# Kernel tuning notes

Measured on AMD Instinct MI355X. Metric: run time of the kernel, lower is better.

Reference implementation:

```python
import jax, jax.numpy as jnp
import numpy as np

NY, NU, NHIDDEN = 64, 64, 256
NHRZ, NBATCH = 1024, 128


def setup_inputs() -> dict:
    key = jax.random.key(0)
    ks = jax.random.split(key, 9)
    y0 = jax.random.normal(ks[0], (NBATCH, NY), dtype=jnp.float32)
    U = jax.random.normal(ks[1], (NHRZ, NBATCH, NU), dtype=jnp.float32)
    # parameters (match torch init: uniform(0,1) for continuous eigen params,
    # randn/sqrt(Nu) for B, Kaiming-uniform-ish for Linear layers)
    lmbd_cont_real = jax.random.uniform(ks[2], (NHIDDEN // 2,), dtype=jnp.float32)
    lmbd_cont_imag = jax.random.uniform(ks[3], (NHIDDEN // 2,), dtype=jnp.float32)
    B = jax.random.normal(ks[4], (NHIDDEN, NU), dtype=jnp.float32) / np.sqrt(NU)
    lim1 = 1.0 / np.sqrt(NY)
    W_y2x = jax.random.uniform(ks[5], (NHIDDEN, NY), dtype=jnp.float32, minval=-lim1, maxval=lim1)
    b_y2x = jax.random.uniform(ks[6], (NHIDDEN,), dtype=jnp.float32, minval=-lim1, maxval=lim1)
    lim2 = 1.0 / np.sqrt(NHIDDEN)
    W_x2y = jax.random.uniform(ks[7], (NY, NHIDDEN), dtype=jnp.float32, minval=-lim2, maxval=lim2)
    b_x2y = jax.random.uniform(ks[8], (NY,), dtype=jnp.float32, minval=-lim2, maxval=lim2)
    return {"y0": y0, "U": U, "lmbd_cont_real": lmbd_cont_real,
            "lmbd_cont_imag": lmbd_cont_imag, "B": B,
            "W_y2x": W_y2x, "b_y2x": b_y2x, "W_x2y": W_x2y, "b_x2y": b_x2y}


def reference(y0, U, lmbd_cont_real, lmbd_cont_imag, B, W_y2x, b_y2x, W_x2y, b_x2y):
    n = lmbd_cont_real.shape[0]  # Nhidden // 2
    r = jnp.exp(-jnp.abs(lmbd_cont_real))
    theta = (np.pi / 2.0) * lmbd_cont_imag
    lmbd_real = r * jnp.cos(theta)  # [n]
    lmbd_imag = r * jnp.sin(theta)  # [n]
    nf = jnp.sqrt(1.0 - jnp.exp(-2.0 * jnp.abs(lmbd_cont_real)))
    nf = jnp.concatenate([nf, nf])  # [Nhidden]
    # Bu[t,b,h] = (U @ B^T) * nf
    Bu = jnp.einsum('tbu,hu->tbh', U, B) * nf  # [Nhrz, Nbatch, Nhidden]
    x0 = y0 @ W_y2x.T + b_y2x  # [Nbatch, Nhidden]

    # x @ A^T with A = [[diag(lr), -diag(li)], [diag(li), diag(lr)]] is a
    # per-pair 2x2 rotation -> pure elementwise ops (same math, no dense matmul)
    def step(x, bu):
        x1, x2 = x[:, :n], x[:, n:]
        xn = jnp.concatenate([lmbd_real * x1 - lmbd_imag * x2,
                              lmbd_imag * x1 + lmbd_real * x2], axis=-1) + bu
        return xn, xn

    _, X = jax.lax.scan(step, x0, Bu)  # X: [Nhrz, Nbatch, Nhidden]
    Y = X @ W_x2y.T + b_x2y  # [Nhrz, Nbatch, Ny]
    return Y
```

## Files before the change

kernel.cpp:

```cpp
#include <hip/hip_runtime.h>
#include <hip/hip_bf16.h>
#include <stdint.h>

#define T_HRZ 1024
#define NBAT  128
#define NHID  256
#define NPAIR 128
#define NUIN  64
#define NYOUT 64
#define LCH   16
#define CCH   64

#define WS_LAM   0
#define WS_LAML  256
#define WS_X0P   512
#define WS_WBU   33280
#define WS_WBY   41472
#define WS_S     49664
#define WS_E     2146816

#define X16_PITCH 264
#define XA_SB 136
#define XA_SK 552

typedef __attribute__((ext_vector_type(8))) short short8;
typedef __attribute__((ext_vector_type(4))) float float4v;

union Frag { short8 s8; unsigned int u32[4]; };

__device__ __forceinline__ unsigned int f2bf_bits(float x) {
  unsigned int u = __float_as_uint(x);
  return (u + 0x7fffu + ((u >> 16) & 1u)) >> 16;
}

__device__ __forceinline__ unsigned int pkbf(float a, float b) {
  __hip_bfloat162 h = __float22bfloat162_rn(make_float2(a, b));
  union { __hip_bfloat162 h2; unsigned int u; } cv; cv.h2 = h; return cv.u;
}

__global__ __launch_bounds__(256) void k_prep(
    const float* __restrict__ y0, const float* __restrict__ lrc,
    const float* __restrict__ lic, const float* __restrict__ Bm,
    const float* __restrict__ Wy2x, const float* __restrict__ by2x,
    const float* __restrict__ Wx2y, float* __restrict__ ws)
{
  int blk = blockIdx.x;
  int h = threadIdx.x;
  if (blk < NBAT) {
    __shared__ float y0s[NYOUT];
    if (h < NYOUT) y0s[h] = y0[blk * NYOUT + h];
    __syncthreads();
    float acc = by2x[h];
    const float* wr = Wy2x + h * NYOUT;
#pragma unroll 16
    for (int k = 0; k < NYOUT; ++k) acc += y0s[k] * wr[k];
    int j = h & (NPAIR - 1);
    int comp = h >> 7;
    ws[WS_X0P + (blk * NPAIR + j) * 2 + comp] = acc;
  } else if (blk == NBAT) {
    if (h < NPAIR) {
      float a  = fabsf(lrc[h]);
      float r  = expf(-a);
      float th = 1.5707963267948966f * lic[h];
      float lr = r * cosf(th);
      float li = r * sinf(th);
      ws[WS_LAM + h]         = lr;
      ws[WS_LAM + NPAIR + h] = li;
      float pr = lr, pi_ = li;
      for (int l = 1; l < LCH; ++l) {
        float nr = pr * lr - pi_ * li;
        float ni = pr * li + pi_ * lr;
        pr = nr; pi_ = ni;
      }
      ws[WS_LAML + h]         = pr;
      ws[WS_LAML + NPAIR + h] = pi_;
    }
  } else if (blk == NBAT + 1) {
    unsigned short* wbu = (unsigned short*)(ws + WS_WBU);
    for (int idx = h; idx < 16384; idx += 256) {
      int nt   = idx >> 10;
      int kk   = (idx >> 9) & 1;
      int lane = (idx >> 3) & 63;
      int jj   = idx & 7;
      int u  = kk * 32 + (lane >> 4) * 8 + jj;
      int hh = nt * 16 + (lane & 15);
      float a2 = fabsf(lrc[hh & (NPAIR - 1)]);
      float nf = sqrtf(1.f - expf(-2.f * a2));
      wbu[idx] = (unsigned short)f2bf_bits(Bm[hh * NUIN + u] * nf);
    }
  } else {
    unsigned short* wby = (unsigned short*)(ws + WS_WBY);
    for (int idx = h; idx < 16384; idx += 256) {
      int nt   = idx >> 12;
      int kk   = (idx >> 9) & 7;
      int lane = (idx >> 3) & 63;
      int jj   = idx & 7;
      int hh = kk * 32 + (lane >> 4) * 8 + jj;
      int y  = nt * 16 + (lane & 15);
      wby[idx] = (unsigned short)f2bf_bits(Wx2y[y * NHID + hh]);
    }
  }
}

__global__ __launch_bounds__(128, 6) void k_phaseA(
    const float* __restrict__ U, float* __restrict__ ws)
{
  int b = blockIdx.x, c = blockIdx.y;
  int tid = threadIdx.x, wave = tid >> 6, lane = tid & 63;
  int l15 = lane & 15, q = lane >> 4;
  __shared__ unsigned short X16[LCH * X16_PITCH];

  const float* urow = U + ((size_t)(c * LCH + l15) * NBAT + b) * NUIN;
  Frag afr[2];
#pragma unroll
  for (int kk = 0; kk < 2; ++kk) {
    int u0 = kk * 32 + q * 8;
    float4 va = *(const float4*)(urow + u0);
    float4 vb = *(const float4*)(urow + u0 + 4);
    afr[kk].u32[0] = pkbf(va.x, va.y);
    afr[kk].u32[1] = pkbf(va.z, va.w);
    afr[kk].u32[2] = pkbf(vb.x, vb.y);
    afr[kk].u32[3] = pkbf(vb.z, vb.w);
  }

  const short8* wbu = (const short8*)(ws + WS_WBU);
  float4v z = {0.f, 0.f, 0.f, 0.f};
  float4v acc[8];
#pragma unroll
  for (int n = 0; n < 8; ++n) acc[n] = z;
#pragma unroll
  for (int n = 0; n < 8; ++n) {
    int nt = wave * 8 + n;
    acc[n] = __builtin_amdgcn_mfma_f32_16x16x32_bf16(afr[0].s8, wbu[(nt * 2 + 0) * 64 + lane], acc[n], 0, 0, 0);
    acc[n] = __builtin_amdgcn_mfma_f32_16x16x32_bf16(afr[1].s8, wbu[(nt * 2 + 1) * 64 + lane], acc[n], 0, 0, 0);
  }

#pragma unroll
  for (int n = 0; n < 8; ++n) {
    int hh = (wave * 8 + n) * 16 + l15;
    int off = (hh & 127) * 2 + (hh >> 7);
#pragma unroll
    for (int r = 0; r < 4; ++r)
      X16[(q * 4 + r) * X16_PITCH + off] = (unsigned short)f2bf_bits(acc[n][r]);
  }
  __syncthreads();

  int j = tid;
  float lr = ws[WS_LAM + j], li = ws[WS_LAM + NPAIR + j];
  unsigned int pk[LCH];
#pragma unroll
  for (int l = 0; l < LCH; ++l)
    pk[l] = *(const unsigned int*)(X16 + l * X16_PITCH + j * 2);
  float s1 = 0.f, s2 = 0.f;
#pragma unroll
  for (int l = 0; l < LCH; ++l) {
    float v1 = __uint_as_float(pk[l] << 16);
    float v2 = __uint_as_float(pk[l] & 0xffff0000u);
    float n1 = lr * s1 - li * s2 + v1;
    float n2 = li * s1 + lr * s2 + v2;
    s1 = n1; s2 = n2;
  }
  ((float2*)(ws + WS_S))[((size_t)c * NBAT + b) * NPAIR + j] = make_float2(s1, s2);
}

__global__ __launch_bounds__(128) void k_phaseB(float* __restrict__ ws)
{
  int b = blockIdx.x, j = threadIdx.x;
  float e1 = ws[WS_X0P + (b * NPAIR + j) * 2 + 0];
  float e2 = ws[WS_X0P + (b * NPAIR + j) * 2 + 1];
  float Lr = ws[WS_LAML + j], Li = ws[WS_LAML + NPAIR + j];
  const float2* sp = (const float2*)(ws + WS_S);
  float2* ep = (float2*)(ws + WS_E);
  const size_t cs = (size_t)NBAT * NPAIR;
  size_t o0 = (size_t)b * NPAIR + j;
  float2 buf[8];
#pragma unroll
  for (int k = 0; k < 8; ++k) buf[k] = sp[k * cs + o0];
  for (int g = 0; g < 8; ++g) {
    float2 nxt[8];
    if (g < 7) {
#pragma unroll
      for (int k = 0; k < 8; ++k) nxt[k] = sp[(size_t)((g + 1) * 8 + k) * cs + o0];
    }
#pragma unroll
    for (int k = 0; k < 8; ++k) {
      ep[(size_t)(g * 8 + k) * cs + o0] = make_float2(e1, e2);
      float n1 = Lr * e1 - Li * e2 + buf[k].x;
      float n2 = Li * e1 + Lr * e2 + buf[k].y;
      e1 = n1; e2 = n2;
    }
    if (g < 7) {
#pragma unroll
      for (int k = 0; k < 8; ++k) buf[k] = nxt[k];
    }
  }
}

__global__ __launch_bounds__(128, 4) void k_phaseC(
    const float* __restrict__ U, const float* __restrict__ bx2y,
    float* __restrict__ out, float* __restrict__ ws)
{
  int b = blockIdx.x, c = blockIdx.y;
  int tid = threadIdx.x, wave = tid >> 6, lane = tid & 63;
  int l15 = lane & 15, q = lane >> 4;
  __shared__ unsigned short X16[LCH * X16_PITCH];
  __shared__ unsigned short XA[8 * XA_SK];

  int j = tid;
  float lr = ws[WS_LAM + j], li = ws[WS_LAM + NPAIR + j];
  float2 e = ((const float2*)(ws + WS_E))[((size_t)c * NBAT + b) * NPAIR + j];

  const float* urow = U + ((size_t)(c * LCH + l15) * NBAT + b) * NUIN;
  Frag afr[2];
#pragma unroll
  for (int kk = 0; kk < 2; ++kk) {
    int u0 = kk * 32 + q * 8;
    float4 va = *(const float4*)(urow + u0);
    float4 vb = *(const float4*)(urow + u0 + 4);
    afr[kk].u32[0] = pkbf(va.x, va.y);
    afr[kk].u32[1] = pkbf(va.z, va.w);
    afr[kk].u32[2] = pkbf(vb.x, vb.y);
    afr[kk].u32[3] = pkbf(vb.z, vb.w);
  }

  const short8* wbu = (const short8*)(ws + WS_WBU);
  float4v z = {0.f, 0.f, 0.f, 0.f};
  {
    float4v acc[8];
#pragma unroll
    for (int n = 0; n < 8; ++n) acc[n] = z;
#pragma unroll
    for (int n = 0; n < 8; ++n) {
      int nt = wave * 8 + n;
      acc[n] = __builtin_amdgcn_mfma_f32_16x16x32_bf16(afr[0].s8, wbu[(nt * 2 + 0) * 64 + lane], acc[n], 0, 0, 0);
      acc[n] = __builtin_amdgcn_mfma_f32_16x16x32_bf16(afr[1].s8, wbu[(nt * 2 + 1) * 64 + lane], acc[n], 0, 0, 0);
    }
#pragma unroll
    for (int n = 0; n < 8; ++n) {
      int hh = (wave * 8 + n) * 16 + l15;
      int off = (hh & 127) * 2 + (hh >> 7);
#pragma unroll
      for (int r = 0; r < 4; ++r)
        X16[(q * 4 + r) * X16_PITCH + off] = (unsigned short)f2bf_bits(acc[n][r]);
    }
  }
  __syncthreads();

  unsigned int pk[LCH];
#pragma unroll
  for (int l = 0; l < LCH; ++l)
    pk[l] = *(const unsigned int*)(X16 + l * X16_PITCH + j * 2);

  int base1 = (j >> 5) * XA_SK       + ((j >> 3) & 3) * XA_SB + (j & 7);
  int base2 = ((j >> 5) + 4) * XA_SK + ((j >> 3) & 3) * XA_SB + (j & 7);
  float x1 = e.x, x2 = e.y;
#pragma unroll
  for (int l = 0; l < LCH; ++l) {
    float v1 = __uint_as_float(pk[l] << 16);
    float v2 = __uint_as_float(pk[l] & 0xffff0000u);
    float n1 = lr * x1 - li * x2 + v1;
    float n2 = li * x1 + lr * x2 + v2;
    x1 = n1; x2 = n2;
    XA[base1 + l * 8] = (unsigned short)f2bf_bits(x1);
    XA[base2 + l * 8] = (unsigned short)f2bf_bits(x2);
  }
  __syncthreads();

  const short8* wby = (const short8*)(ws + WS_WBY);
  float4v acc0 = z, acc1 = z;
  int nt0 = wave * 2, nt1 = nt0 + 1;
#pragma unroll
  for (int kk = 0; kk < 8; ++kk) {
    short8 a = *(const short8*)(XA + kk * XA_SK + q * XA_SB + l15 * 8);
    acc0 = __builtin_amdgcn_mfma_f32_16x16x32_bf16(a, wby[(nt0 * 8 + kk) * 64 + lane], acc0, 0, 0, 0);
    acc1 = __builtin_amdgcn_mfma_f32_16x16x32_bf16(a, wby[(nt1 * 8 + kk) * 64 + lane], acc1, 0, 0, 0);
  }

  float bias0 = bx2y[nt0 * 16 + l15];
  float bias1 = bx2y[nt1 * 16 + l15];
#pragma unroll
  for (int r = 0; r < 4; ++r) {
    int row = q * 4 + r;
    size_t o = ((size_t)(c * LCH + row) * NBAT + b) * NYOUT;
    out[o + nt0 * 16 + l15] = acc0[r] + bias0;
    out[o + nt1 * 16 + l15] = acc1[r] + bias1;
  }
}

extern "C" void kernel_launch(void* const* d_in, const int* in_sizes, int n_in,
                              void* d_out, int out_size, void* d_ws, size_t ws_size,
                              hipStream_t stream) {
  (void)in_sizes; (void)n_in; (void)out_size; (void)ws_size;
  const float* y0   = (const float*)d_in[0];
  const float* U    = (const float*)d_in[1];
  const float* lrc  = (const float*)d_in[2];
  const float* lic  = (const float*)d_in[3];
  const float* Bm   = (const float*)d_in[4];
  const float* Wy2x = (const float*)d_in[5];
  const float* by2x = (const float*)d_in[6];
  const float* Wx2y = (const float*)d_in[7];
  const float* bx2y = (const float*)d_in[8];
  float* out = (float*)d_out;
  float* ws  = (float*)d_ws;

  k_prep<<<dim3(NBAT + 3), 256, 0, stream>>>(y0, lrc, lic, Bm, Wy2x, by2x, Wx2y, ws);
  k_phaseA<<<dim3(NBAT, CCH), 128, 0, stream>>>(U, ws);
  k_phaseB<<<dim3(NBAT), 128, 0, stream>>>(ws);
  k_phaseC<<<dim3(NBAT, CCH), 128, 0, stream>>>(U, bx2y, out, ws);
}
```

Before: 154.3 us.

## Make phase A/C blocks persistent over 16 batches with prefetched U loads

Phase A and C kernels change from one 128-thread block per (batch, chunk) to 512 blocks of 256 threads. Each block handles two batches at a time and loops over 16 batches of a chunk, prefetching the next U rows and E carry into registers while computing the current ones. The aim is to cut block-launch overhead and hide global load latency by double-buffering in registers. The cost is fewer blocks (512 vs 8192), which lowers parallelism, plus extra __syncthreads per iteration and higher register pressure.

After: 162.9 us. 5.6% more time.

```diff
diff --git a/kernel.cpp b/kernel.cpp
--- a/kernel.cpp
+++ b/kernel.cpp
@@ -102,65 +102,82 @@
   }
 }
 
-__global__ __launch_bounds__(128, 6) void k_phaseA(
+__global__ __launch_bounds__(256, 2) void k_phaseA(
     const float* __restrict__ U, float* __restrict__ ws)
 {
-  int b = blockIdx.x, c = blockIdx.y;
-  int tid = threadIdx.x, wave = tid >> 6, lane = tid & 63;
-  int l15 = lane & 15, q = lane >> 4;
-  __shared__ unsigned short X16[LCH * X16_PITCH];
-
-  const float* urow = U + ((size_t)(c * LCH + l15) * NBAT + b) * NUIN;
-  Frag afr[2];
-#pragma unroll
-  for (int kk = 0; kk < 2; ++kk) {
-    int u0 = kk * 32 + q * 8;
-    float4 va = *(const float4*)(urow + u0);
-    float4 vb = *(const float4*)(urow + u0 + 4);
-    afr[kk].u32[0] = pkbf(va.x, va.y);
-    afr[kk].u32[1] = pkbf(va.z, va.w);
-    afr[kk].u32[2] = pkbf(vb.x, vb.y);
-    afr[kk].u32[3] = pkbf(vb.z, vb.w);
-  }
-
+  const int bid = blockIdx.x, tid = threadIdx.x;
+  __shared__ unsigned short X16[2][LCH * X16_PITCH];
+
+  const int c  = bid >> 3;
+  const int b0 = (bid & 7) << 4;
+  const int w = tid >> 6, lane = tid & 63;
+  const int wt = w & 1;
+  const int tg = w >> 1;
+  const int l15 = lane & 15, q = lane >> 4;
+  const int g = tid >> 7;
+  const int jscan = tid & 127;
+
+  const float lr = ws[WS_LAM + jscan], li = ws[WS_LAM + NPAIR + jscan];
   const short8* wbu = (const short8*)(ws + WS_WBU);
-  float4v z = {0.f, 0.f, 0.f, 0.f};
-  float4v acc[8];
-#pragma unroll
-  for (int n = 0; n < 8; ++n) acc[n] = z;
-#pragma unroll
-  for (int n = 0; n < 8; ++n) {
-    int nt = wave * 8 + n;
-    acc[n] = __builtin_amdgcn_mfma_f32_16x16x32_bf16(afr[0].s8, wbu[(nt * 2 + 0) * 64 + lane], acc[n], 0, 0, 0);
-    acc[n] = __builtin_amdgcn_mfma_f32_16x16x32_bf16(afr[1].s8, wbu[(nt * 2 + 1) * 64 + lane], acc[n], 0, 0, 0);
-  }
-
-#pragma unroll
-  for (int n = 0; n < 8; ++n) {
-    int hh = (wave * 8 + n) * 16 + l15;
-    int off = (hh & 127) * 2 + (hh >> 7);
-#pragma unroll
-    for (int r = 0; r < 4; ++r)
-      X16[(q * 4 + r) * X16_PITCH + off] = (unsigned short)f2bf_bits(acc[n][r]);
-  }
-  __syncthreads();
-
-  int j = tid;
-  float lr = ws[WS_LAM + j], li = ws[WS_LAM + NPAIR + j];
-  unsigned int pk[LCH];
-#pragma unroll
-  for (int l = 0; l < LCH; ++l)
-    pk[l] = *(const unsigned int*)(X16 + l * X16_PITCH + j * 2);
-  float s1 = 0.f, s2 = 0.f;
-#pragma unroll
-  for (int l = 0; l < LCH; ++l) {
-    float v1 = __uint_as_float(pk[l] << 16);
-    float v2 = __uint_as_float(pk[l] & 0xffff0000u);
-    float n1 = lr * s1 - li * s2 + v1;
-    float n2 = li * s1 + lr * s2 + v2;
-    s1 = n1; s2 = n2;
-  }
-  ((float2*)(ws + WS_S))[((size_t)c * NBAT + b) * NPAIR + j] = make_float2(s1, s2);
+  const float4v z = {0.f, 0.f, 0.f, 0.f};
+  float2* Sp = (float2*)(ws + WS_S);
+
+  float4 cur0, cur1, cur2, cur3, nxt0, nxt1, nxt2, nxt3;
+  {
+    const float* p = U + ((size_t)(c * LCH + l15) * NBAT + (b0 + tg)) * NUIN + q * 8;
+    cur0 = *(const float4*)(p);      cur1 = *(const float4*)(p + 4);
+    cur2 = *(const float4*)(p + 32); cur3 = *(const float4*)(p + 36);
+  }
+#pragma unroll
+  for (int i = 0; i < 8; ++i) {
+    if (i < 7) {
+      const float* p = U + ((size_t)(c * LCH + l15) * NBAT + (b0 + 2 * (i + 1) + tg)) * NUIN + q * 8;
+      nxt0 = *(const float4*)(p);      nxt1 = *(const float4*)(p + 4);
+      nxt2 = *(const float4*)(p + 32); nxt3 = *(const float4*)(p + 36);
+    }
+    Frag afr[2];
+    afr[0].u32[0] = pkbf(cur0.x, cur0.y); afr[0].u32[1] = pkbf(cur0.z, cur0.w);
+    afr[0].u32[2] = pkbf(cur1.x, cur1.y); afr[0].u32[3] = pkbf(cur1.z, cur1.w);
+    afr[1].u32[0] = pkbf(cur2.x, cur2.y); afr[1].u32[1] = pkbf(cur2.z, cur2.w);
+    afr[1].u32[2] = pkbf(cur3.x, cur3.y); afr[1].u32[3] = pkbf(cur3.z, cur3.w);
+
+    float4v acc[8];
+#pragma unroll
+    for (int n = 0; n < 8; ++n) acc[n] = z;
+#pragma unroll
+    for (int n = 0; n < 8; ++n) {
+      int nt = wt * 8 + n;
+      acc[n] = __builtin_amdgcn_mfma_f32_16x16x32_bf16(afr[0].s8, wbu[(nt * 2 + 0) * 64 + lane], acc[n], 0, 0, 0);
+      acc[n] = __builtin_amdgcn_mfma_f32_16x16x32_bf16(afr[1].s8, wbu[(nt * 2 + 1) * 64 + lane], acc[n], 0, 0, 0);
+    }
+#pragma unroll
+    for (int n = 0; n < 8; ++n) {
+      int hh = (wt * 8 + n) * 16 + l15;
+      int off = (hh & 127) * 2 + (hh >> 7);
+#pragma unroll
+      for (int r = 0; r < 4; ++r)
+        X16[tg][(q * 4 + r) * X16_PITCH + off] = (unsigned short)f2bf_bits(acc[n][r]);
+    }
+    __syncthreads();
+
+    unsigned int pk[LCH];
+#pragma unroll
+    for (int l = 0; l < LCH; ++l)
+      pk[l] = *(const unsigned int*)(&X16[g][l * X16_PITCH + jscan * 2]);
+    float s1 = 0.f, s2 = 0.f;
+#pragma unroll
+    for (int l = 0; l < LCH; ++l) {
+      float v1 = __uint_as_float(pk[l] << 16);
+      float v2 = __uint_as_float(pk[l] & 0xffff0000u);
+      float n1 = lr * s1 - li * s2 + v1;
+      float n2 = li * s1 + lr * s2 + v2;
+      s1 = n1; s2 = n2;
+    }
+    int bs = b0 + 2 * i + g;
+    Sp[((size_t)c * NBAT + bs) * NPAIR + jscan] = make_float2(s1, s2);
+    __syncthreads();
+    if (i < 7) { cur0 = nxt0; cur1 = nxt1; cur2 = nxt2; cur3 = nxt3; }
+  }
 }
 
 __global__ __launch_bounds__(128) void k_phaseB(float* __restrict__ ws)
@@ -196,94 +213,109 @@
   }
 }
 
-__global__ __launch_bounds__(128, 4) void k_phaseC(
+__global__ __launch_bounds__(256, 2) void k_phaseC(
     const float* __restrict__ U, const float* __restrict__ bx2y,
     float* __restrict__ out, float* __restrict__ ws)
 {
-  int b = blockIdx.x, c = blockIdx.y;
-  int tid = threadIdx.x, wave = tid >> 6, lane = tid & 63;
-  int l15 = lane & 15, q = lane >> 4;
-  __shared__ unsigned short X16[LCH * X16_PITCH];
-  __shared__ unsigned short XA[8 * XA_SK];
-
-  int j = tid;
-  float lr = ws[WS_LAM + j], li = ws[WS_LAM + NPAIR + j];
-  float2 e = ((const float2*)(ws + WS_E))[((size_t)c * NBAT + b) * NPAIR + j];
-
-  const float* urow = U + ((size_t)(c * LCH + l15) * NBAT + b) * NUIN;
-  Frag afr[2];
-#pragma unroll
-  for (int kk = 0; kk < 2; ++kk) {
-    int u0 = kk * 32 + q * 8;
-    float4 va = *(const float4*)(urow + u0);
-    float4 vb = *(const float4*)(urow + u0 + 4);
-    afr[kk].u32[0] = pkbf(va.x, va.y);
-    afr[kk].u32[1] = pkbf(va.z, va.w);
-    afr[kk].u32[2] = pkbf(vb.x, vb.y);
-    afr[kk].u32[3] = pkbf(vb.z, vb.w);
-  }
-
+  const int bid = blockIdx.x, tid = threadIdx.x;
+  __shared__ unsigned short X16[2][LCH * X16_PITCH];
+  __shared__ unsigned short XA[2][8 * XA_SK];
+
+  const int c  = bid >> 3;
+  const int b0 = (bid & 7) << 4;
+  const int w = tid >> 6, lane = tid & 63;
+  const int wt = w & 1;
+  const int tg = w >> 1;
+  const int l15 = lane & 15, q = lane >> 4;
+  const int g = tid >> 7;
+  const int jscan = tid & 127;
+
+  const float lr = ws[WS_LAM + jscan], li = ws[WS_LAM + NPAIR + jscan];
   const short8* wbu = (const short8*)(ws + WS_WBU);
-  float4v z = {0.f, 0.f, 0.f, 0.f};
+  const short8* wby = (const short8*)(ws + WS_WBY);
+  const float2* Ep = (const float2*)(ws + WS_E);
+  const float4v z = {0.f, 0.f, 0.f, 0.f};
+  const int nt0 = wt * 2, nt1 = nt0 + 1;
+  const float bias0 = bx2y[nt0 * 16 + l15];
+  const float bias1 = bx2y[nt1 * 16 + l15];
+  const int base1 = (jscan >> 5) * XA_SK + ((jscan >> 3) & 3) * XA_SB + (jscan & 7);
+  const int base2 = ((jscan >> 5) + 4) * XA_SK + ((jscan >> 3) & 3) * XA_SB + (jscan & 7);
+
+  float4 cur0, cur1, cur2, cur3, nxt0, nxt1, nxt2, nxt3;
+  float2 ec, en;
   {
+    const float* p = U + ((size_t)(c * LCH + l15) * NBAT + (b0 + tg)) * NUIN + q * 8;
+    cur0 = *(const float4*)(p);      cur1 = *(const float4*)(p + 4);
+    cur2 = *(const float4*)(p + 32); cur3 = *(const float4*)(p + 36);
+    ec = Ep[((size_t)c * NBAT + (b0 + g)) * NPAIR + jscan];
+  }
+#pragma unroll
+  for (int i = 0; i < 8; ++i) {
+    if (i < 7) {
+      const float* p = U + ((size_t)(c * LCH + l15) * NBAT + (b0 + 2 * (i + 1) + tg)) * NUIN + q * 8;
+      nxt0 = *(const float4*)(p);      nxt1 = *(const float4*)(p + 4);
+      nxt2 = *(const float4*)(p + 32); nxt3 = *(const float4*)(p + 36);
+      en = Ep[((size_t)c * NBAT + (b0 + 2 * (i + 1) + g)) * NPAIR + jscan];
+    }
+    Frag afr[2];
+    afr[0].u32[0] = pkbf(cur0.x, cur0.y); afr[0].u32[1] = pkbf(cur0.z, cur0.w);
+    afr[0].u32[2] = pkbf(cur1.x, cur1.y); afr[0].u32[3] = pkbf(cur1.z, cur1.w);
+    afr[1].u32[0] = pkbf(cur2.x, cur2.y); afr[1].u32[1] = pkbf(cur2.z, cur2.w);
+    afr[1].u32[2] = pkbf(cur3.x, cur3.y); afr[1].u32[3] = pkbf(cur3.z, cur3.w);
+
     float4v acc[8];
 #pragma unroll
     for (int n = 0; n < 8; ++n) acc[n] = z;
 #pragma unroll
     for (int n = 0; n < 8; ++n) {
-      int nt = wave * 8 + n;
+      int nt = wt * 8 + n;
       acc[n] = __builtin_amdgcn_mfma_f32_16x16x32_bf16(afr[0].s8, wbu[(nt * 2 + 0) * 64 + lane], acc[n], 0, 0, 0);
       acc[n] = __builtin_amdgcn_mfma_f32_16x16x32_bf16(afr[1].s8, wbu[(nt * 2 + 1) * 64 + lane], acc[n], 0, 0, 0);
     }
 #pragma unroll
     for (int n = 0; n < 8; ++n) {
-      int hh = (wave * 8 + n) * 16 + l15;
+      int hh = (wt * 8 + n) * 16 + l15;
       int off = (hh & 127) * 2 + (hh >> 7);
 #pragma unroll
       for (int r = 0; r < 4; ++r)
-        X16[(q * 4 + r) * X16_PITCH + off] = (unsigned short)f2bf_bits(acc[n][r]);
-    }
-  }
-  __syncthreads();
-
-  unsigned int pk[LCH];
-#pragma unroll
-  for (int l = 0; l < LCH; ++l)
-    pk[l] = *(const unsigned int*)(X16 + l * X16_PITCH + j * 2);
-
-  int base1 = (j >> 5) * XA_SK       + ((j >> 3) & 3) * XA_SB + (j & 7);
-  int base2 = ((j >> 5) + 4) * XA_SK + ((j >> 3) & 3) * XA_SB + (j & 7);
-  float x1 = e.x, x2 = e.y;
-#pragma unroll
-  for (int l = 0; l < LCH; ++l) {
-    float v1 = __uint_as_float(pk[l] << 16);
-    float v2 = __uint_as_float(pk[l] & 0xffff0000u);
-    float n1 = lr * x1 - li * x2 + v1;
-    float n2 = li * x1 + lr * x2 + v2;
-    x1 = n1; x2 = n2;
-    XA[base1 + l * 8] = (unsigned short)f2bf_bits(x1);
-    XA[base2 + l * 8] = (unsigned short)f2bf_bits(x2);
-  }
-  __syncthreads();
-
-  const short8* wby = (const short8*)(ws + WS_WBY);
-  float4v acc0 = z, acc1 = z;
-  int nt0 = wave * 2, nt1 = nt0 + 1;
-#pragma unroll
-  for (int kk = 0; kk < 8; ++kk) {
-    short8 a = *(const short8*)(XA + kk * XA_SK + q * XA_SB + l15 * 8);
-    acc0 = __builtin_amdgcn_mfma_f32_16x16x32_bf16(a, wby[(nt0 * 8 + kk) * 64 + lane], acc0, 0, 0, 0);
-    acc1 = __builtin_amdgcn_mfma_f32_16x16x32_bf16(a, wby[(nt1 * 8 + kk) * 64 + lane], acc1, 0, 0, 0);
-  }
-
-  float bias0 = bx2y[nt0 * 16 + l15];
-  float bias1 = bx2y[nt1 * 16 + l15];
-#pragma unroll
-  for (int r = 0; r < 4; ++r) {
-    int row = q * 4 + r;
-    size_t o = ((size_t)(c * LCH + row) * NBAT + b) * NYOUT;
-    out[o + nt0 * 16 + l15] = acc0[r] + bias0;
-    out[o + nt1 * 16 + l15] = acc1[r] + bias1;
+        X16[tg][(q * 4 + r) * X16_PITCH + off] = (unsigned short)f2bf_bits(acc[n][r]);
+    }
+    __syncthreads();
+
+    unsigned int pk[LCH];
+#pragma unroll
+    for (int l = 0; l < LCH; ++l)
+      pk[l] = *(const unsigned int*)(&X16[g][l * X16_PITCH + jscan * 2]);
+    float x1 = ec.x, x2 = ec.y;
+#pragma unroll
+    for (int l = 0; l < LCH; ++l) {
+      float v1 = __uint_as_float(pk[l] << 16);
+      float v2 = __uint_as_float(pk[l] & 0xffff0000u);
+      float n1 = lr * x1 - li * x2 + v1;
+      float n2 = li * x1 + lr * x2 + v2;
+      x1 = n1; x2 = n2;
+      XA[g][base1 + l * 8] = (unsigned short)f2bf_bits(x1);
+      XA[g][base2 + l * 8] = (unsigned short)f2bf_bits(x2);
+    }
+    __syncthreads();
+
+    float4v acc0 = z, acc1 = z;
+#pragma unroll
+    for (int kk = 0; kk < 8; ++kk) {
+      short8 a = *(const short8*)(&XA[tg][kk * XA_SK + q * XA_SB + l15 * 8]);
+      acc0 = __builtin_amdgcn_mfma_f32_16x16x32_bf16(a, wby[(nt0 * 8 + kk) * 64 + lane], acc0, 0, 0, 0);
+      acc1 = __builtin_amdgcn_mfma_f32_16x16x32_bf16(a, wby[(nt1 * 8 + kk) * 64 + lane], acc1, 0, 0, 0);
+    }
+    int bm = b0 + 2 * i + tg;
+#pragma unroll
+    for (int r = 0; r < 4; ++r) {
+      int row = q * 4 + r;
+      size_t o = ((size_t)(c * LCH + row) * NBAT + bm) * NYOUT;
+      out[o + nt0 * 16 + l15] = acc0[r] + bias0;
+      out[o + nt1 * 16 + l15] = acc1[r] + bias1;
+    }
+    __syncthreads();
+    if (i < 7) { cur0 = nxt0; cur1 = nxt1; cur2 = nxt2; cur3 = nxt3; ec = en; }
   }
 }
 
@@ -304,7 +336,7 @@
   float* ws  = (float*)d_ws;
 
   k_prep<<<dim3(NBAT + 3), 256, 0, stream>>>(y0, lrc, lic, Bm, Wy2x, by2x, Wx2y, ws);
-  k_phaseA<<<dim3(NBAT, CCH), 128, 0, stream>>>(U, ws);
+  k_phaseA<<<dim3(512), 256, 0, stream>>>(U, ws);
   k_phaseB<<<dim3(NBAT), 128, 0, stream>>>(ws);
-  k_phaseC<<<dim3(NBAT, CCH), 128, 0, stream>>>(U, bx2y, out, ws);
-}
+  k_phaseC<<<dim3(512), 256, 0, stream>>>(U, bx2y, out, ws);
+}
```

## Scan chunks in MFMA registers via shuffle prefix, drop LDS staging

Applied to the files above, without the earlier changes.

Phase A and phase C no longer round-trip the Bu chunk through a bf16 LDS buffer. Each lane now runs a 4-step local recurrence over its MFMA accumulator rows, and the four lane groups are combined with a shuffle-based prefix scan that uses precomputed lambda powers (L^4, L^8). Phase C builds the MFMA A operand for the output projection straight from registers into a swizzled LDS layout, and W_x2y is re-permuted to match the interleaved pair ordering. This removes one LDS pass, one barrier and the sequential 16-step per-thread scan. It adds shuffles, more registers (occupancy hints lowered) and slightly different rounding, since Bu is no longer rounded to bf16 before the scan.

Result: slower. 157.9 us (+2.3%).

```diff
diff --git a/kernel.cpp b/kernel.cpp
--- a/kernel.cpp
+++ b/kernel.cpp
@@ -18,10 +18,6 @@
 #define WS_WBY   41472
 #define WS_S     49664
 #define WS_E     2146816
-
-#define X16_PITCH 264
-#define XA_SB 136
-#define XA_SK 552
 
 typedef __attribute__((ext_vector_type(8))) short short8;
 typedef __attribute__((ext_vector_type(4))) float float4v;
@@ -95,72 +91,76 @@
       int kk   = (idx >> 9) & 7;
       int lane = (idx >> 3) & 63;
       int jj   = idx & 7;
-      int hh = kk * 32 + (lane >> 4) * 8 + jj;
+      int k  = kk * 32 + ((lane >> 4) & 3) * 8 + jj;
+      int hh = (k >> 1) + (k & 1) * NPAIR;
       int y  = nt * 16 + (lane & 15);
       wby[idx] = (unsigned short)f2bf_bits(Wx2y[y * NHID + hh]);
     }
   }
 }
 
-__global__ __launch_bounds__(128, 6) void k_phaseA(
+__global__ __launch_bounds__(128, 4) void k_phaseA(
     const float* __restrict__ U, float* __restrict__ ws)
 {
-  int b = blockIdx.x, c = blockIdx.y;
-  int tid = threadIdx.x, wave = tid >> 6, lane = tid & 63;
-  int l15 = lane & 15, q = lane >> 4;
-  __shared__ unsigned short X16[LCH * X16_PITCH];
-
-  const float* urow = U + ((size_t)(c * LCH + l15) * NBAT + b) * NUIN;
+  const int b = blockIdx.x, c = blockIdx.y;
+  const int tid = threadIdx.x, wt = tid >> 6, lane = tid & 63;
+  const int l15 = lane & 15, q = lane >> 4;
+
+  const float* urow = U + ((size_t)(c * LCH + l15) * NBAT + b) * NUIN + q * 8;
+  float4 u0 = *(const float4*)(urow);
+  float4 u1 = *(const float4*)(urow + 4);
+  float4 u2 = *(const float4*)(urow + 32);
+  float4 u3 = *(const float4*)(urow + 36);
+
+  float lrv[4], liv[4];
+#pragma unroll
+  for (int p = 0; p < 4; ++p) {
+    int j = wt * 64 + p * 16 + l15;
+    lrv[p] = ws[WS_LAM + j];
+    liv[p] = ws[WS_LAM + NPAIR + j];
+  }
+
   Frag afr[2];
-#pragma unroll
-  for (int kk = 0; kk < 2; ++kk) {
-    int u0 = kk * 32 + q * 8;
-    float4 va = *(const float4*)(urow + u0);
-    float4 vb = *(const float4*)(urow + u0 + 4);
-    afr[kk].u32[0] = pkbf(va.x, va.y);
-    afr[kk].u32[1] = pkbf(va.z, va.w);
-    afr[kk].u32[2] = pkbf(vb.x, vb.y);
-    afr[kk].u32[3] = pkbf(vb.z, vb.w);
-  }
+  afr[0].u32[0] = pkbf(u0.x, u0.y); afr[0].u32[1] = pkbf(u0.z, u0.w);
+  afr[0].u32[2] = pkbf(u1.x, u1.y); afr[0].u32[3] = pkbf(u1.z, u1.w);
+  afr[1].u32[0] = pkbf(u2.x, u2.y); afr[1].u32[1] = pkbf(u2.z, u2.w);
+  afr[1].u32[2] = pkbf(u3.x, u3.y); afr[1].u32[3] = pkbf(u3.z, u3.w);
 
   const short8* wbu = (const short8*)(ws + WS_WBU);
-  float4v z = {0.f, 0.f, 0.f, 0.f};
-  float4v acc[8];
-#pragma unroll
-  for (int n = 0; n < 8; ++n) acc[n] = z;
-#pragma unroll
-  for (int n = 0; n < 8; ++n) {
-    int nt = wave * 8 + n;
-    acc[n] = __builtin_amdgcn_mfma_f32_16x16x32_bf16(afr[0].s8, wbu[(nt * 2 + 0) * 64 + lane], acc[n], 0, 0, 0);
-    acc[n] = __builtin_amdgcn_mfma_f32_16x16x32_bf16(afr[1].s8, wbu[(nt * 2 + 1) * 64 + lane], acc[n], 0, 0, 0);
-  }
-
-#pragma unroll
-  for (int n = 0; n < 8; ++n) {
-    int hh = (wave * 8 + n) * 16 + l15;
-    int off = (hh & 127) * 2 + (hh >> 7);
-#pragma unroll
-    for (int r = 0; r < 4; ++r)
-      X16[(q * 4 + r) * X16_PITCH + off] = (unsigned short)f2bf_bits(acc[n][r]);
-  }
-  __syncthreads();
-
-  int j = tid;
-  float lr = ws[WS_LAM + j], li = ws[WS_LAM + NPAIR + j];
-  unsigned int pk[LCH];
-#pragma unroll
-  for (int l = 0; l < LCH; ++l)
-    pk[l] = *(const unsigned int*)(X16 + l * X16_PITCH + j * 2);
-  float s1 = 0.f, s2 = 0.f;
-#pragma unroll
-  for (int l = 0; l < LCH; ++l) {
-    float v1 = __uint_as_float(pk[l] << 16);
-    float v2 = __uint_as_float(pk[l] & 0xffff0000u);
-    float n1 = lr * s1 - li * s2 + v1;
-    float n2 = li * s1 + lr * s2 + v2;
-    s1 = n1; s2 = n2;
-  }
-  ((float2*)(ws + WS_S))[((size_t)c * NBAT + b) * NPAIR + j] = make_float2(s1, s2);
+  const float4v z = {0.f, 0.f, 0.f, 0.f};
+  float4v accLo[4], accHi[4];
+#pragma unroll
+  for (int p = 0; p < 4; ++p) { accLo[p] = z; accHi[p] = z; }
+#pragma unroll
+  for (int p = 0; p < 4; ++p) {
+    int ntLo = wt * 4 + p, ntHi = ntLo + 8;
+    accLo[p] = __builtin_amdgcn_mfma_f32_16x16x32_bf16(afr[0].s8, wbu[(ntLo * 2 + 0) * 64 + lane], accLo[p], 0, 0, 0);
+    accLo[p] = __builtin_amdgcn_mfma_f32_16x16x32_bf16(afr[1].s8, wbu[(ntLo * 2 + 1) * 64 + lane], accLo[p], 0, 0, 0);
+    accHi[p] = __builtin_amdgcn_mfma_f32_16x16x32_bf16(afr[0].s8, wbu[(ntHi * 2 + 0) * 64 + lane], accHi[p], 0, 0, 0);
+    accHi[p] = __builtin_amdgcn_mfma_f32_16x16x32_bf16(afr[1].s8, wbu[(ntHi * 2 + 1) * 64 + lane], accHi[p], 0, 0, 0);
+  }
+
+  float2* Sp = (float2*)(ws + WS_S);
+#pragma unroll
+  for (int p = 0; p < 4; ++p) {
+    float lr = lrv[p], li = liv[p];
+    float s1 = accLo[p][0], s2 = accHi[p][0];
+#pragma unroll
+    for (int r = 1; r < 4; ++r) {
+      float n1 = lr * s1 - li * s2 + accLo[p][r];
+      float n2 = li * s1 + lr * s2 + accHi[p][r];
+      s1 = n1; s2 = n2;
+    }
+    float l2r = lr * lr - li * li,      l2i = 2.f * lr * li;
+    float L4r = l2r * l2r - l2i * l2i,  L4i = 2.f * l2r * l2i;
+    float L8r = L4r * L4r - L4i * L4i,  L8i = 2.f * L4r * L4i;
+    float t1 = __shfl_up(s1, 16), t2 = __shfl_up(s2, 16);
+    if (q >= 1) { float n1 = s1 + L4r * t1 - L4i * t2, n2 = s2 + L4i * t1 + L4r * t2; s1 = n1; s2 = n2; }
+    t1 = __shfl_up(s1, 32); t2 = __shfl_up(s2, 32);
+    if (q >= 2) { float n1 = s1 + L8r * t1 - L8i * t2, n2 = s2 + L8i * t1 + L8r * t2; s1 = n1; s2 = n2; }
+    if (q == 3)
+      Sp[((size_t)c * NBAT + b) * NPAIR + wt * 64 + p * 16 + l15] = make_float2(s1, s2);
+  }
 }
 
 __global__ __launch_bounds__(128) void k_phaseB(float* __restrict__ ws)
@@ -196,82 +196,99 @@
   }
 }
 
-__global__ __launch_bounds__(128, 4) void k_phaseC(
+__global__ __launch_bounds__(128, 3) void k_phaseC(
     const float* __restrict__ U, const float* __restrict__ bx2y,
     float* __restrict__ out, float* __restrict__ ws)
 {
-  int b = blockIdx.x, c = blockIdx.y;
-  int tid = threadIdx.x, wave = tid >> 6, lane = tid & 63;
-  int l15 = lane & 15, q = lane >> 4;
-  __shared__ unsigned short X16[LCH * X16_PITCH];
-  __shared__ unsigned short XA[8 * XA_SK];
-
-  int j = tid;
-  float lr = ws[WS_LAM + j], li = ws[WS_LAM + NPAIR + j];
-  float2 e = ((const float2*)(ws + WS_E))[((size_t)c * NBAT + b) * NPAIR + j];
-
-  const float* urow = U + ((size_t)(c * LCH + l15) * NBAT + b) * NUIN;
+  const int b = blockIdx.x, c = blockIdx.y;
+  const int tid = threadIdx.x, wt = tid >> 6, lane = tid & 63;
+  const int l15 = lane & 15, q = lane >> 4;
+  __shared__ unsigned short XAs[8 * 64 * 8];
+
+  const float* urow = U + ((size_t)(c * LCH + l15) * NBAT + b) * NUIN + q * 8;
+  float4 u0 = *(const float4*)(urow);
+  float4 u1 = *(const float4*)(urow + 4);
+  float4 u2 = *(const float4*)(urow + 32);
+  float4 u3 = *(const float4*)(urow + 36);
+
+  const float2* Ep = (const float2*)(ws + WS_E);
+  float lrv[4], liv[4]; float2 ev[4];
+#pragma unroll
+  for (int p = 0; p < 4; ++p) {
+    int j = wt * 64 + p * 16 + l15;
+    lrv[p] = ws[WS_LAM + j];
+    liv[p] = ws[WS_LAM + NPAIR + j];
+    ev[p]  = Ep[((size_t)c * NBAT + b) * NPAIR + j];
+  }
+
   Frag afr[2];
-#pragma unroll
-  for (int kk = 0; kk < 2; ++kk) {
-    int u0 = kk * 32 + q * 8;
-    float4 va = *(const float4*)(urow + u0);
-    float4 vb = *(const float4*)(urow + u0 + 4);
-    afr[kk].u32[0] = pkbf(va.x, va.y);
-    afr[kk].u32[1] = pkbf(va.z, va.w);
-    afr[kk].u32[2] = pkbf(vb.x, vb.y);
-    afr[kk].u32[3] = pkbf(vb.z, vb.w);
-  }
+  afr[0].u32[0] = pkbf(u0.x, u0.y); afr[0].u32[1] = pkbf(u0.z, u0.w);
+  afr[0].u32[2] = pkbf(u1.x, u1.y); afr[0].u32[3] = pkbf(u1.z, u1.w);
+  afr[1].u32[0] = pkbf(u2.x, u2.y); afr[1].u32[1] = pkbf(u2.z, u2.w);
+  afr[1].u32[2] = pkbf(u3.x, u3.y); afr[1].u32[3] = pkbf(u3.z, u3.w);
 
   const short8* wbu = (const short8*)(ws + WS_WBU);
-  float4v z = {0.f, 0.f, 0.f, 0.f};
-  {
-    float4v acc[8];
-#pragma unroll
-    for (int n = 0; n < 8; ++n) acc[n] = z;
-#pragma unroll
-    for (int n = 0; n < 8; ++n) {
-      int nt = wave * 8 + n;
-      acc[n] = __builtin_amdgcn_mfma_f32_16x16x32_bf16(afr[0].s8, wbu[(nt * 2 + 0) * 64 + lane], acc[n], 0, 0, 0);
-      acc[n] = __builtin_amdgcn_mfma_f32_16x16x32_bf16(afr[1].s8, wbu[(nt * 2 + 1) * 64 + lane], acc[n], 0, 0, 0);
-    }
-#pragma unroll
-    for (int n = 0; n < 8; ++n) {
-      int hh = (wave * 8 + n) * 16 + l15;
-      int off = (hh & 127) * 2 + (hh >> 7);
-#pragma unroll
-      for (int r = 0; r < 4; ++r)
-        X16[(q * 4 + r) * X16_PITCH + off] = (unsigned short)f2bf_bits(acc[n][r]);
-    }
-  }
-  __syncthreads();
-
-  unsigned int pk[LCH];
-#pragma unroll
-  for (int l = 0; l < LCH; ++l)
-    pk[l] = *(const unsigned int*)(X16 + l * X16_PITCH + j * 2);
-
-  int base1 = (j >> 5) * XA_SK       + ((j >> 3) & 3) * XA_SB + (j & 7);
-  int base2 = ((j >> 5) + 4) * XA_SK + ((j >> 3) & 3) * XA_SB + (j & 7);
-  float x1 = e.x, x2 = e.y;
-#pragma unroll
-  for (int l = 0; l < LCH; ++l) {
-    float v1 = __uint_as_float(pk[l] << 16);
-    float v2 = __uint_as_float(pk[l] & 0xffff0000u);
-    float n1 = lr * x1 - li * x2 + v1;
-    float n2 = li * x1 + lr * x2 + v2;
-    x1 = n1; x2 = n2;
-    XA[base1 + l * 8] = (unsigned short)f2bf_bits(x1);
-    XA[base2 + l * 8] = (unsigned short)f2bf_bits(x2);
+  const float4v z = {0.f, 0.f, 0.f, 0.f};
+  float4v accLo[4], accHi[4];
+#pragma unroll
+  for (int p = 0; p < 4; ++p) { accLo[p] = z; accHi[p] = z; }
+#pragma unroll
+  for (int p = 0; p < 4; ++p) {
+    int ntLo = wt * 4 + p, ntHi = ntLo + 8;
+    accLo[p] = __builtin_amdgcn_mfma_f32_16x16x32_bf16(afr[0].s8, wbu[(ntLo * 2 + 0) * 64 + lane], accLo[p], 0, 0, 0);
+    accLo[p] = __builtin_amdgcn_mfma_f32_16x16x32_bf16(afr[1].s8, wbu[(ntLo * 2 + 1) * 64 + lane], accLo[p], 0, 0, 0);
+    accHi[p] = __builtin_amdgcn_mfma_f32_16x16x32_bf16(afr[0].s8, wbu[(ntHi * 2 + 0) * 64 + lane], accHi[p], 0, 0, 0);
+    accHi[p] = __builtin_amdgcn_mfma_f32_16x16x32_bf16(afr[1].s8, wbu[(ntHi * 2 + 1) * 64 + lane], accHi[p], 0, 0, 0);
+  }
+
+#pragma unroll
+  for (int p = 0; p < 4; ++p) {
+    float lr = lrv[p], li = liv[p];
+    float s1 = 0.f, s2 = 0.f;
+#pragma unroll
+    for (int r = 0; r < 4; ++r) {
+      float n1 = lr * s1 - li * s2 + accLo[p][r];
+      float n2 = li * s1 + lr * s2 + accHi[p][r];
+      s1 = n1; s2 = n2;
+      accLo[p][r] = s1; accHi[p][r] = s2;
+    }
+    float l2r = lr * lr - li * li,      l2i = 2.f * lr * li;
+    float L4r = l2r * l2r - l2i * l2i,  L4i = 2.f * l2r * l2i;
+    float L8r = L4r * L4r - L4i * L4i,  L8i = 2.f * L4r * L4i;
+    float t1 = __shfl_up(s1, 16), t2 = __shfl_up(s2, 16);
+    if (q >= 1) { float n1 = s1 + L4r * t1 - L4i * t2, n2 = s2 + L4i * t1 + L4r * t2; s1 = n1; s2 = n2; }
+    t1 = __shfl_up(s1, 32); t2 = __shfl_up(s2, 32);
+    if (q >= 2) { float n1 = s1 + L8r * t1 - L8i * t2, n2 = s2 + L8i * t1 + L8r * t2; s1 = n1; s2 = n2; }
+    float P1 = __shfl_up(s1, 16), P2 = __shfl_up(s2, 16);
+    if (q == 0) { P1 = 0.f; P2 = 0.f; }
+    float e1 = ev[p].x, e2 = ev[p].y;
+    if (q & 1) { float n1 = L4r * e1 - L4i * e2, n2 = L4i * e1 + L4r * e2; e1 = n1; e2 = n2; }
+    if (q & 2) { float n1 = L8r * e1 - L8i * e2, n2 = L8i * e1 + L8r * e2; e1 = n1; e2 = n2; }
+    float T1 = P1 + e1, T2 = P2 + e2;
+    float m1 = lr * T1 - li * T2, m2 = li * T1 + lr * T2;
+    int kk = wt * 4 + p;
+    int laneBase = (l15 >> 2) * 16 + q * 4;
+    int jj = (l15 & 3) * 2;
+#pragma unroll
+    for (int r = 0; r < 4; ++r) {
+      float x1 = accLo[p][r] + m1;
+      float x2 = accHi[p][r] + m2;
+      int lp = laneBase + r;
+      int g  = kk * 64 + lp;
+      int addr = ((g ^ (lp >> 3)) << 3) + jj;
+      *(unsigned int*)(&XAs[addr]) = f2bf_bits(x1) | (f2bf_bits(x2) << 16);
+      if (r < 3) { float n1 = lr * m1 - li * m2; m2 = li * m1 + lr * m2; m1 = n1; }
+    }
   }
   __syncthreads();
 
   const short8* wby = (const short8*)(ws + WS_WBY);
   float4v acc0 = z, acc1 = z;
-  int nt0 = wave * 2, nt1 = nt0 + 1;
+  const int nt0 = wt * 2, nt1 = nt0 + 1;
 #pragma unroll
   for (int kk = 0; kk < 8; ++kk) {
-    short8 a = *(const short8*)(XA + kk * XA_SK + q * XA_SB + l15 * 8);
+    int g = kk * 64 + lane;
+    short8 a = *(const short8*)(&XAs[(size_t)((g ^ (lane >> 3)) << 3)]);
     acc0 = __builtin_amdgcn_mfma_f32_16x16x32_bf16(a, wby[(nt0 * 8 + kk) * 64 + lane], acc0, 0, 0, 0);
     acc1 = __builtin_amdgcn_mfma_f32_16x16x32_bf16(a, wby[(nt1 * 8 + kk) * 64 + lane], acc1, 0, 0, 0);
   }
```
